# Kernel tuning notes

Measured on AMD Instinct MI355X. Metric: run time of the kernel, lower is better.

The kernel has to match this reference:

```python
import jax, jax.numpy as jnp
import numpy as np

V = 200000  # number of variables (fixed num_segments for aggregation)


def setup_inputs() -> dict:
    key = jax.random.key(0)
    ks = jax.random.split(key, 10)
    E, D, Fe, P = 1000000, 128, 16, 2
    Hm, Hag, Ha = 256, 256, 256  # mem_hidden, mem_agg_hidden, agg_hidden
    Din = D + Fe + 1

    def w(k, shape):
        return jax.random.normal(k, shape, jnp.float32) / jnp.sqrt(shape[1])

    return {
        "variable_state": jax.random.normal(ks[0], (E, D), jnp.float32),
        "edge_feature": jax.random.normal(ks[1], (E, Fe), jnp.float32),
        "solution": jax.random.uniform(ks[2], (V,), jnp.float32),
        "W1m": w(ks[3], (Hm, Din)), "b1m": jnp.zeros((Hm,), jnp.float32),
        "W2m": w(ks[4], (Hag, Hm)),
        "W1a": w(ks[5], (Ha, Hag)), "b1a": jnp.zeros((Ha,), jnp.float32),
        "W2a": w(ks[6], (D, Ha)),
        "Wc": w(ks[7], (P, D)), "bc": jnp.zeros((P,), jnp.float32),
        "variable_index": jax.random.randint(ks[8], (E,), 0, V, jnp.int32),
        "edge_sign": 2 * jax.random.randint(ks[9], (E,), 0, 2, jnp.int32) - 1,
    }


def reference(variable_state, edge_feature, solution, W1m, b1m, W2m, W1a, b1a,
              W2a, Wc, bc, variable_index, edge_sign):
    ls = jax.nn.log_sigmoid
    # per-edge signed solution column: mm(signed_mask, solution) on the sparse incidence
    signed = (edge_sign.astype(jnp.float32) * solution[variable_index])[:, None]  # [E,1]
    x = jnp.concatenate([variable_state, edge_feature, signed], axis=1)  # [E, Din]
    # memory MLP: Linear -> logsigmoid -> Linear -> logsigmoid
    s = ls(ls(x @ W1m.T + b1m) @ W2m.T)  # [E, Hag]
    # aggregation mm(variable_mask, state): sum edges per variable
    agg = jax.ops.segment_sum(s, variable_index, num_segments=V)  # [V, Hag]
    # aggregator MLP
    h = ls(ls(agg @ W1a.T + b1a) @ W2a.T)  # [V, D]
    # variable classifier
    return h @ Wc.T + bc  # [V, P]
```

## Files before the change

### kernel.cpp

```cpp
#include <hip/hip_runtime.h>
#include <hip/hip_bf16.h>

typedef unsigned short u16;
typedef __attribute__((ext_vector_type(8))) short   short8;
typedef __attribute__((ext_vector_type(8))) __bf16  bf16x8;
typedef __attribute__((ext_vector_type(16))) float  floatx16;

#define DD  128
#define FE  16
#define DIN 145
#define K1  160
#define K1P 168
#define HQ  256
#define HQP 264
#define ME  64
#define MV  32

__device__ __forceinline__ float logsig(float x) {
    return fminf(x, 0.f) - __logf(1.f + __expf(-fabsf(x)));
}
__device__ __forceinline__ u16 f2b(float f) {
    union { float f; unsigned u; } x; x.f = f;
    unsigned r = x.u + 0x7fffu + ((x.u >> 16) & 1u);
    return (u16)(r >> 16);
}
__device__ __forceinline__ ushort4 f2b4(float4 v) {
    ushort4 o; o.x = f2b(v.x); o.y = f2b(v.y); o.z = f2b(v.z); o.w = f2b(v.w);
    return o;
}
__device__ __forceinline__ bf16x8 ld_bf8_lds(const short* p) {
    return __builtin_bit_cast(bf16x8, *(const short8*)p);
}
__device__ __forceinline__ bf16x8 ld_bf8_glb(const short* p) {
    return __builtin_bit_cast(bf16x8, *(const short8*)p);
}

__global__ __launch_bounds__(256) void conv_weights(
    const float* __restrict__ W1m, const float* __restrict__ W2m,
    const float* __restrict__ W1a, const float* __restrict__ W2a,
    short* __restrict__ W1mb, short* __restrict__ W2mb,
    short* __restrict__ W1ab, short* __restrict__ W2ab)
{
    int i = blockIdx.x * 256 + threadIdx.x;
    if (i < 256 * K1) {
        int n = i / K1, k = i - n * K1;
        W1mb[i] = (k < DIN) ? (short)f2b(W1m[n * DIN + k]) : (short)0;
    } else if (i < 256 * K1 + 256 * HQ) {
        int j = i - 256 * K1;
        W2mb[j] = (short)f2b(W2m[j]);
    } else if (i < 256 * K1 + 2 * 256 * HQ) {
        int j = i - 256 * K1 - 256 * HQ;
        W1ab[j] = (short)f2b(W1a[j]);
    } else if (i < 256 * K1 + 2 * 256 * HQ + 128 * HQ) {
        int j = i - 256 * K1 - 2 * 256 * HQ;
        W2ab[j] = (short)f2b(W2a[j]);
    }
}

__global__ __launch_bounds__(256) void edge_mfma(
    const float* __restrict__ vs, const float* __restrict__ ef,
    const float* __restrict__ sol, const float* __restrict__ b1m,
    const short* __restrict__ W1mb, const short* __restrict__ W2mb,
    const int* __restrict__ vidx, const int* __restrict__ esign,
    float* __restrict__ agg, int E)
{
    __shared__ short xs[ME][K1P];
    __shared__ short h1s[ME][HQP];
    __shared__ int   vix[ME];
    const int tid = threadIdx.x;
    const int e0 = blockIdx.x * ME;

    for (int i = tid; i < ME * 32; i += 256) {
        int e = i >> 5, q = (i & 31) << 2;
        float4 v = *(const float4*)&vs[(size_t)(e0 + e) * DD + q];
        *(ushort4*)&xs[e][q] = f2b4(v);
    }
    for (int i = tid; i < ME * 4; i += 256) {
        int e = i >> 2, q = (i & 3) << 2;
        float4 v = *(const float4*)&ef[(size_t)(e0 + e) * FE + q];
        *(ushort4*)&xs[e][DD + q] = f2b4(v);
    }
    for (int i = tid; i < ME * 16; i += 256) {
        int e = i >> 4, k = i & 15;
        if (k == 0) {
            int gi = vidx[e0 + e];
            vix[e] = gi;
            xs[e][144] = (short)f2b((float)esign[e0 + e] * sol[gi]);
        } else {
            xs[e][144 + k] = 0;
        }
    }
    __syncthreads();

    const int wv = tid >> 6, lane = tid & 63;
    const int lr = lane & 31, lh = lane >> 5;
    const int n0 = wv * 64;

    floatx16 a00 = {}, a01 = {}, a10 = {}, a11 = {};
    #pragma unroll
    for (int ks = 0; ks < K1 / 16; ++ks) {
        int k = ks * 16 + lh * 8;
        bf16x8 A0 = ld_bf8_lds(&xs[lr][k]);
        bf16x8 A1 = ld_bf8_lds(&xs[32 + lr][k]);
        bf16x8 B0 = ld_bf8_glb(&W1mb[(size_t)(n0 + lr) * K1 + k]);
        bf16x8 B1 = ld_bf8_glb(&W1mb[(size_t)(n0 + 32 + lr) * K1 + k]);
        a00 = __builtin_amdgcn_mfma_f32_32x32x16_bf16(A0, B0, a00, 0, 0, 0);
        a01 = __builtin_amdgcn_mfma_f32_32x32x16_bf16(A0, B1, a01, 0, 0, 0);
        a10 = __builtin_amdgcn_mfma_f32_32x32x16_bf16(A1, B0, a10, 0, 0, 0);
        a11 = __builtin_amdgcn_mfma_f32_32x32x16_bf16(A1, B1, a11, 0, 0, 0);
    }
    {
        float bn0 = b1m[n0 + lr], bn1 = b1m[n0 + 32 + lr];
        #pragma unroll
        for (int r = 0; r < 16; ++r) {
            int row = (r & 3) + 8 * (r >> 2) + 4 * lh;
            h1s[row][n0 + lr]           = (short)f2b(logsig(a00[r] + bn0));
            h1s[row][n0 + 32 + lr]      = (short)f2b(logsig(a01[r] + bn1));
            h1s[32 + row][n0 + lr]      = (short)f2b(logsig(a10[r] + bn0));
            h1s[32 + row][n0 + 32 + lr] = (short)f2b(logsig(a11[r] + bn1));
        }
    }
    __syncthreads();

    a00 = (floatx16){}; a01 = (floatx16){}; a10 = (floatx16){}; a11 = (floatx16){};
    #pragma unroll
    for (int ks = 0; ks < HQ / 16; ++ks) {
        int k = ks * 16 + lh * 8;
        bf16x8 A0 = ld_bf8_lds(&h1s[lr][k]);
        bf16x8 A1 = ld_bf8_lds(&h1s[32 + lr][k]);
        bf16x8 B0 = ld_bf8_glb(&W2mb[(size_t)(n0 + lr) * HQ + k]);
        bf16x8 B1 = ld_bf8_glb(&W2mb[(size_t)(n0 + 32 + lr) * HQ + k]);
        a00 = __builtin_amdgcn_mfma_f32_32x32x16_bf16(A0, B0, a00, 0, 0, 0);
        a01 = __builtin_amdgcn_mfma_f32_32x32x16_bf16(A0, B1, a01, 0, 0, 0);
        a10 = __builtin_amdgcn_mfma_f32_32x32x16_bf16(A1, B0, a10, 0, 0, 0);
        a11 = __builtin_amdgcn_mfma_f32_32x32x16_bf16(A1, B1, a11, 0, 0, 0);
    }
    #pragma unroll
    for (int r = 0; r < 16; ++r) {
        int row = (r & 3) + 8 * (r >> 2) + 4 * lh;
        int va = vix[row], vb = vix[32 + row];
        atomicAdd(&agg[(size_t)va * HQ + n0 + lr],      logsig(a00[r]));
        atomicAdd(&agg[(size_t)va * HQ + n0 + 32 + lr], logsig(a01[r]));
        atomicAdd(&agg[(size_t)vb * HQ + n0 + lr],      logsig(a10[r]));
        atomicAdd(&agg[(size_t)vb * HQ + n0 + 32 + lr], logsig(a11[r]));
    }
}

__global__ __launch_bounds__(256) void var_mfma(
    const float* __restrict__ agg, const float* __restrict__ b1a,
    const short* __restrict__ W1ab, const short* __restrict__ W2ab,
    const float* __restrict__ Wc, const float* __restrict__ bc,
    float* __restrict__ out, int V)
{
    __shared__ short as_s[MV][HQP];
    __shared__ short h1v[MV][HQP];
    __shared__ float hsv[MV][DD + 4];
    const int tid = threadIdx.x;
    const int v0 = blockIdx.x * MV;

    for (int i = tid; i < MV * 64; i += 256) {
        int v = i >> 6, q = (i & 63) << 2;
        float4 a = *(const float4*)&agg[(size_t)(v0 + v) * HQ + q];
        *(ushort4*)&as_s[v][q] = f2b4(a);
    }
    __syncthreads();

    const int wv = tid >> 6, lane = tid & 63;
    const int lr = lane & 31, lh = lane >> 5;
    const int n0 = wv * 64;

    floatx16 c0 = {}, c1 = {};
    #pragma unroll
    for (int ks = 0; ks < HQ / 16; ++ks) {
        int k = ks * 16 + lh * 8;
        bf16x8 A  = ld_bf8_lds(&as_s[lr][k]);
        bf16x8 B0 = ld_bf8_glb(&W1ab[(size_t)(n0 + lr) * HQ + k]);
        bf16x8 B1 = ld_bf8_glb(&W1ab[(size_t)(n0 + 32 + lr) * HQ + k]);
        c0 = __builtin_amdgcn_mfma_f32_32x32x16_bf16(A, B0, c0, 0, 0, 0);
        c1 = __builtin_amdgcn_mfma_f32_32x32x16_bf16(A, B1, c1, 0, 0, 0);
    }
    {
        float bn0 = b1a[n0 + lr], bn1 = b1a[n0 + 32 + lr];
        #pragma unroll
        for (int r = 0; r < 16; ++r) {
            int row = (r & 3) + 8 * (r >> 2) + 4 * lh;
            h1v[row][n0 + lr]      = (short)f2b(logsig(c0[r] + bn0));
            h1v[row][n0 + 32 + lr] = (short)f2b(logsig(c1[r] + bn1));
        }
    }
    __syncthreads();

    floatx16 d0 = {};
    const int n0b = wv * 32;
    #pragma unroll
    for (int ks = 0; ks < HQ / 16; ++ks) {
        int k = ks * 16 + lh * 8;
        bf16x8 A = ld_bf8_lds(&h1v[lr][k]);
        bf16x8 B = ld_bf8_glb(&W2ab[(size_t)(n0b + lr) * HQ + k]);
        d0 = __builtin_amdgcn_mfma_f32_32x32x16_bf16(A, B, d0, 0, 0, 0);
    }
    #pragma unroll
    for (int r = 0; r < 16; ++r) {
        int row = (r & 3) + 8 * (r >> 2) + 4 * lh;
        hsv[row][n0b + lr] = logsig(d0[r]);
    }
    __syncthreads();

    if (tid < MV * 2) {
        int v = tid >> 1, p = tid & 1;
        const float* wrow = Wc + (size_t)p * DD;
        float acc = bc[p];
        for (int k = 0; k < DD; k += 4) {
            float4 w4 = *(const float4*)&wrow[k];
            float4 h4 = *(const float4*)&hsv[v][k];
            acc = fmaf(w4.w, h4.w, fmaf(w4.z, h4.z, fmaf(w4.y, h4.y, fmaf(w4.x, h4.x, acc))));
        }
        out[(size_t)(v0 + v) * 2 + p] = acc;
    }
}

extern "C" void kernel_launch(void* const* d_in, const int* in_sizes, int n_in,
                              void* d_out, int out_size, void* d_ws, size_t ws_size,
                              hipStream_t stream) {
    const float* vs  = (const float*)d_in[0];
    const float* ef  = (const float*)d_in[1];
    const float* sol = (const float*)d_in[2];
    const float* W1m = (const float*)d_in[3];
    const float* b1m = (const float*)d_in[4];
    const float* W2m = (const float*)d_in[5];
    const float* W1a = (const float*)d_in[6];
    const float* b1a = (const float*)d_in[7];
    const float* W2a = (const float*)d_in[8];
    const float* Wc  = (const float*)d_in[9];
    const float* bc  = (const float*)d_in[10];
    const int* vidx  = (const int*)d_in[11];
    const int* sgn   = (const int*)d_in[12];

    const int E = in_sizes[0] / DD;
    const int V = in_sizes[2];

    char* ws = (char*)d_ws;
    float* agg = (float*)ws;
    size_t off = (size_t)V * HQ * sizeof(float);
    short* W1mb = (short*)(ws + off); off += (size_t)256 * K1 * 2;
    short* W2mb = (short*)(ws + off); off += (size_t)256 * HQ * 2;
    short* W1ab = (short*)(ws + off); off += (size_t)256 * HQ * 2;
    short* W2ab = (short*)(ws + off);

    hipMemsetAsync(agg, 0, (size_t)V * HQ * sizeof(float), stream);
    conv_weights<<<dim3(800), dim3(256), 0, stream>>>(
        W1m, W2m, W1a, W2a, W1mb, W2mb, W1ab, W2ab);
    edge_mfma<<<dim3(E / ME), dim3(256), 0, stream>>>(
        vs, ef, sol, b1m, W1mb, W2mb, vidx, sgn, agg, E);
    var_mfma<<<dim3(V / MV), dim3(256), 0, stream>>>(
        agg, b1a, W1ab, W2ab, Wc, bc, (float*)d_out, V);
}
```

Before: 1.769 ms.

## Halve edge tile to 32 rows and parallelize classifier dot across lanes

The edge kernel now processes 32 edges per block instead of 64, with each wave computing a single 32-row MFMA tile. This cuts LDS use and registers for more occupancy, but each block now re-reads the full weight matrices for half as many edges. The variable kernel drops its fp32 staging buffer and stores the final hidden activations as bf16 in the reused input buffer. The classifier dot product is split across four lanes with a shuffle reduction, adding extra rounding of h to bf16 before the classifier.

```diff
diff --git a/kernel.cpp b/kernel.cpp
--- a/kernel.cpp
+++ b/kernel.cpp
@@ -13,7 +13,7 @@
 #define K1P 168
 #define HQ  256
 #define HQP 264
-#define ME  64
+#define ME  32
 #define MV  32
 
 __device__ __forceinline__ float logsig(float x) {
@@ -28,10 +28,7 @@
     ushort4 o; o.x = f2b(v.x); o.y = f2b(v.y); o.z = f2b(v.z); o.w = f2b(v.w);
     return o;
 }
-__device__ __forceinline__ bf16x8 ld_bf8_lds(const short* p) {
-    return __builtin_bit_cast(bf16x8, *(const short8*)p);
-}
-__device__ __forceinline__ bf16x8 ld_bf8_glb(const short* p) {
+__device__ __forceinline__ bf16x8 ld_bf8(const short* p) {
     return __builtin_bit_cast(bf16x8, *(const short8*)p);
 }
 
@@ -75,8 +72,8 @@
         float4 v = *(const float4*)&vs[(size_t)(e0 + e) * DD + q];
         *(ushort4*)&xs[e][q] = f2b4(v);
     }
-    for (int i = tid; i < ME * 4; i += 256) {
-        int e = i >> 2, q = (i & 3) << 2;
+    if (tid < ME * 4) {
+        int e = tid >> 2, q = (tid & 3) << 2;
         float4 v = *(const float4*)&ef[(size_t)(e0 + e) * FE + q];
         *(ushort4*)&xs[e][DD + q] = f2b4(v);
     }
@@ -96,53 +93,43 @@
     const int lr = lane & 31, lh = lane >> 5;
     const int n0 = wv * 64;
 
-    floatx16 a00 = {}, a01 = {}, a10 = {}, a11 = {};
+    floatx16 a0 = {}, a1 = {};
     #pragma unroll
     for (int ks = 0; ks < K1 / 16; ++ks) {
         int k = ks * 16 + lh * 8;
-        bf16x8 A0 = ld_bf8_lds(&xs[lr][k]);
-        bf16x8 A1 = ld_bf8_lds(&xs[32 + lr][k]);
-        bf16x8 B0 = ld_bf8_glb(&W1mb[(size_t)(n0 + lr) * K1 + k]);
-        bf16x8 B1 = ld_bf8_glb(&W1mb[(size_t)(n0 + 32 + lr) * K1 + k]);
-        a00 = __builtin_amdgcn_mfma_f32_32x32x16_bf16(A0, B0, a00, 0, 0, 0);
-        a01 = __builtin_amdgcn_mfma_f32_32x32x16_bf16(A0, B1, a01, 0, 0, 0);
-        a10 = __builtin_amdgcn_mfma_f32_32x32x16_bf16(A1, B0, a10, 0, 0, 0);
-        a11 = __builtin_amdgcn_mfma_f32_32x32x16_bf16(A1, B1, a11, 0, 0, 0);
+        bf16x8 A  = ld_bf8(&xs[lr][k]);
+        bf16x8 B0 = ld_bf8(&W1mb[(size_t)(n0 + lr) * K1 + k]);
+        bf16x8 B1 = ld_bf8(&W1mb[(size_t)(n0 + 32 + lr) * K1 + k]);
+        a0 = __builtin_amdgcn_mfma_f32_32x32x16_bf16(A, B0, a0, 0, 0, 0);
+        a1 = __builtin_amdgcn_mfma_f32_32x32x16_bf16(A, B1, a1, 0, 0, 0);
     }
     {
         float bn0 = b1m[n0 + lr], bn1 = b1m[n0 + 32 + lr];
         #pragma unroll
         for (int r = 0; r < 16; ++r) {
             int row = (r & 3) + 8 * (r >> 2) + 4 * lh;
-            h1s[row][n0 + lr]           = (short)f2b(logsig(a00[r] + bn0));
-            h1s[row][n0 + 32 + lr]      = (short)f2b(logsig(a01[r] + bn1));
-            h1s[32 + row][n0 + lr]      = (short)f2b(logsig(a10[r] + bn0));
-            h1s[32 + row][n0 + 32 + lr] = (short)f2b(logsig(a11[r] + bn1));
-        }
-    }
-    __syncthreads();
-
-    a00 = (floatx16){}; a01 = (floatx16){}; a10 = (floatx16){}; a11 = (floatx16){};
+            h1s[row][n0 + lr]      = (short)f2b(logsig(a0[r] + bn0));
+            h1s[row][n0 + 32 + lr] = (short)f2b(logsig(a1[r] + bn1));
+        }
+    }
+    __syncthreads();
+
+    a0 = (floatx16){}; a1 = (floatx16){};
     #pragma unroll
     for (int ks = 0; ks < HQ / 16; ++ks) {
         int k = ks * 16 + lh * 8;
-        bf16x8 A0 = ld_bf8_lds(&h1s[lr][k]);
-        bf16x8 A1 = ld_bf8_lds(&h1s[32 + lr][k]);
-        bf16x8 B0 = ld_bf8_glb(&W2mb[(size_t)(n0 + lr) * HQ + k]);
-        bf16x8 B1 = ld_bf8_glb(&W2mb[(size_t)(n0 + 32 + lr) * HQ + k]);
-        a00 = __builtin_amdgcn_mfma_f32_32x32x16_bf16(A0, B0, a00, 0, 0, 0);
-        a01 = __builtin_amdgcn_mfma_f32_32x32x16_bf16(A0, B1, a01, 0, 0, 0);
-        a10 = __builtin_amdgcn_mfma_f32_32x32x16_bf16(A1, B0, a10, 0, 0, 0);
-        a11 = __builtin_amdgcn_mfma_f32_32x32x16_bf16(A1, B1, a11, 0, 0, 0);
+        bf16x8 A  = ld_bf8(&h1s[lr][k]);
+        bf16x8 B0 = ld_bf8(&W2mb[(size_t)(n0 + lr) * HQ + k]);
+        bf16x8 B1 = ld_bf8(&W2mb[(size_t)(n0 + 32 + lr) * HQ + k]);
+        a0 = __builtin_amdgcn_mfma_f32_32x32x16_bf16(A, B0, a0, 0, 0, 0);
+        a1 = __builtin_amdgcn_mfma_f32_32x32x16_bf16(A, B1, a1, 0, 0, 0);
     }
     #pragma unroll
     for (int r = 0; r < 16; ++r) {
         int row = (r & 3) + 8 * (r >> 2) + 4 * lh;
-        int va = vix[row], vb = vix[32 + row];
-        atomicAdd(&agg[(size_t)va * HQ + n0 + lr],      logsig(a00[r]));
-        atomicAdd(&agg[(size_t)va * HQ + n0 + 32 + lr], logsig(a01[r]));
-        atomicAdd(&agg[(size_t)vb * HQ + n0 + lr],      logsig(a10[r]));
-        atomicAdd(&agg[(size_t)vb * HQ + n0 + 32 + lr], logsig(a11[r]));
+        int va = vix[row];
+        atomicAdd(&agg[(size_t)va * HQ + n0 + lr],      logsig(a0[r]));
+        atomicAdd(&agg[(size_t)va * HQ + n0 + 32 + lr], logsig(a1[r]));
     }
 }
 
@@ -154,7 +141,6 @@
 {
     __shared__ short as_s[MV][HQP];
     __shared__ short h1v[MV][HQP];
-    __shared__ float hsv[MV][DD + 4];
     const int tid = threadIdx.x;
     const int v0 = blockIdx.x * MV;
 
@@ -173,9 +159,9 @@
     #pragma unroll
     for (int ks = 0; ks < HQ / 16; ++ks) {
         int k = ks * 16 + lh * 8;
-        bf16x8 A  = ld_bf8_lds(&as_s[lr][k]);
-        bf16x8 B0 = ld_bf8_glb(&W1ab[(size_t)(n0 + lr) * HQ + k]);
-        bf16x8 B1 = ld_bf8_glb(&W1ab[(size_t)(n0 + 32 + lr) * HQ + k]);
+        bf16x8 A  = ld_bf8(&as_s[lr][k]);
+        bf16x8 B0 = ld_bf8(&W1ab[(size_t)(n0 + lr) * HQ + k]);
+        bf16x8 B1 = ld_bf8(&W1ab[(size_t)(n0 + 32 + lr) * HQ + k]);
         c0 = __builtin_amdgcn_mfma_f32_32x32x16_bf16(A, B0, c0, 0, 0, 0);
         c1 = __builtin_amdgcn_mfma_f32_32x32x16_bf16(A, B1, c1, 0, 0, 0);
     }
@@ -195,27 +181,35 @@
     #pragma unroll
     for (int ks = 0; ks < HQ / 16; ++ks) {
         int k = ks * 16 + lh * 8;
-        bf16x8 A = ld_bf8_lds(&h1v[lr][k]);
-        bf16x8 B = ld_bf8_glb(&W2ab[(size_t)(n0b + lr) * HQ + k]);
+        bf16x8 A = ld_bf8(&h1v[lr][k]);
+        bf16x8 B = ld_bf8(&W2ab[(size_t)(n0b + lr) * HQ + k]);
         d0 = __builtin_amdgcn_mfma_f32_32x32x16_bf16(A, B, d0, 0, 0, 0);
     }
+    __syncthreads();
     #pragma unroll
     for (int r = 0; r < 16; ++r) {
         int row = (r & 3) + 8 * (r >> 2) + 4 * lh;
-        hsv[row][n0b + lr] = logsig(d0[r]);
-    }
-    __syncthreads();
-
-    if (tid < MV * 2) {
-        int v = tid >> 1, p = tid & 1;
-        const float* wrow = Wc + (size_t)p * DD;
-        float acc = bc[p];
-        for (int k = 0; k < DD; k += 4) {
-            float4 w4 = *(const float4*)&wrow[k];
-            float4 h4 = *(const float4*)&hsv[v][k];
-            acc = fmaf(w4.w, h4.w, fmaf(w4.z, h4.z, fmaf(w4.y, h4.y, fmaf(w4.x, h4.x, acc))));
-        }
-        out[(size_t)(v0 + v) * 2 + p] = acc;
+        as_s[row][n0b + lr] = (short)f2b(logsig(d0[r]));
+    }
+    __syncthreads();
+
+    {
+        int oid = tid >> 2;
+        int part = tid & 3;
+        int v = oid >> 1, p = oid & 1;
+        const float* wrow = Wc + (size_t)p * DD + part * 32;
+        const short* hrow = &as_s[v][part * 32];
+        float acc = 0.f;
+        #pragma unroll
+        for (int k = 0; k < 32; k += 8) {
+            bf16x8 h8 = ld_bf8(&hrow[k]);
+            #pragma unroll
+            for (int j = 0; j < 8; ++j)
+                acc = fmaf((float)h8[j], wrow[k + j], acc);
+        }
+        acc += __shfl_down(acc, 1);
+        acc += __shfl_down(acc, 2);
+        if (part == 0) out[(size_t)(v0 + v) * 2 + p] = acc + bc[p];
     }
 }
 
```

Result: slower. 1.963 ms (+11.0%).
